# Kernel tuning notes

Measured on AMD Instinct MI355X. Metric: run time of the kernel, lower is better.

The kernel has to match this reference:

```python
import jax, jax.numpy as jnp
import numpy as np

N = 8192
E = 262144
NFEAT = 200
NHID = 128
NOUT = 16
CLUSTERS = (10, 5)


def _layernorm(x, g, b, eps=1e-5):
    mu = jnp.mean(x, axis=-1, keepdims=True)
    var = jnp.var(x, axis=-1, keepdims=True)
    return (x - mu) / jnp.sqrt(var + eps) * g + b


def _gumbel_softmax_hard(logits, g, tau=1.0):
    # straight-through gumbel softmax (hard=True), dim=1
    y = jax.nn.softmax((logits + g) / tau, axis=1)
    hard = jax.nn.one_hot(jnp.argmax(y, axis=1), y.shape[1], dtype=y.dtype)
    return hard + y - jax.lax.stop_gradient(y)


def _row_normalize(x, eps=1e-12):
    n = jnp.linalg.norm(x, axis=1, keepdims=True)
    return x / jnp.maximum(n, eps)


def setup_inputs() -> dict:
    key = jax.random.key(0)
    ks = jax.random.split(key, 20)
    u0 = jax.random.uniform(ks[3], (N, CLUSTERS[0]), minval=1e-6, maxval=1.0 - 1e-6)
    u1 = jax.random.uniform(ks[4], (CLUSTERS[0], CLUSTERS[1]), minval=1e-6, maxval=1.0 - 1e-6)
    s = 0.05
    return {
        'x': jax.random.normal(ks[0], (N, NFEAT), dtype=jnp.float32),
        'edge_index': jax.random.randint(ks[1], (2, E), 0, N, dtype=jnp.int32),
        'edge_weight': jax.random.uniform(ks[2], (E,), dtype=jnp.float32),
        'gumbel0': -jnp.log(-jnp.log(u0)),
        'gumbel1': -jnp.log(-jnp.log(u1)),
        # GCN params (2 layers, layernorm)
        'Wg1': jax.random.normal(ks[5], (NHID, NFEAT)) * s,
        'bg1': jnp.zeros((NHID,)),
        'ln1_g': jnp.ones((NHID,)), 'ln1_b': jnp.zeros((NHID,)),
        'Wg2': jax.random.normal(ks[6], (NHID, NHID)) * s,
        'bg2': jnp.zeros((NHID,)),
        'ln2_g': jnp.ones((NHID,)), 'ln2_b': jnp.zeros((NHID,)),
        # per-level pool + encoder linears
        'pool0_W': jax.random.normal(ks[7], (CLUSTERS[0], NHID)) * s,
        'pool0_b': jnp.zeros((CLUSTERS[0],)),
        'pool1_W': jax.random.normal(ks[8], (CLUSTERS[1], NHID)) * s,
        'pool1_b': jnp.zeros((CLUSTERS[1],)),
        'enc0_W': jax.random.normal(ks[9], (NHID, NHID)) * s,
        'enc0_b': jnp.zeros((NHID,)),
        'enc1_W': jax.random.normal(ks[10], (NHID, NHID)) * s,
        'enc1_b': jnp.zeros((NHID,)),
        'fc_W': jax.random.normal(ks[11], (NOUT, 3 * NHID)) * s,
        'fc_b': jnp.zeros((NOUT,)),
    }


def reference(x, edge_index, edge_weight, gumbel0, gumbel1,
              Wg1, bg1, ln1_g, ln1_b, Wg2, bg2, ln2_g, ln2_b,
              pool0_W, pool0_b, pool1_W, pool1_b,
              enc0_W, enc0_b, enc1_W, enc1_b, fc_W, fc_b):
    src, dst = edge_index[0], edge_index[1]

    def agg(h):  # weighted neighbor sum: out[i] = sum_{e: dst_e=i} w_e * h[src_e]
        return jax.ops.segment_sum(h[src] * edge_weight[:, None], dst, num_segments=N)

    # bottom GCN encoder (2 layers, layernorm)
    h = agg(x) @ Wg1.T + bg1
    h = jax.nn.relu(_layernorm(h, ln1_g, ln1_b))
    h = agg(h) @ Wg2.T + bg2
    h = _layernorm(h, ln2_g, ln2_b)
    latent = jax.nn.relu(h)  # [N, nhid]
    all_latents = [latent]

    # dense adjacency (to_dense_adj)
    adj = jnp.zeros((N, N), dtype=x.dtype).at[src, dst].add(edge_weight)

    pools = [(pool0_W, pool0_b), (pool1_W, pool1_b)]
    encs = [(enc0_W, enc0_b), (enc1_W, enc1_b)]
    gumbels = [gumbel0, gumbel1]
    product = None
    for level in range(len(CLUSTERS)):
        pW, pb = pools[level]
        eW, eb = encs[level]
        assign = _gumbel_softmax_hard(latent @ pW.T + pb, gumbels[level])  # [n_l, K]
        product = assign if level == 0 else product @ assign  # [N, K]
        xc = _row_normalize(assign.T @ latent)  # [K, nhid]
        adj = assign.T @ adj @ assign  # [K, K]
        adj = adj / jnp.sum(adj + 1e-8)
        latent = jax.nn.relu((adj @ xc) @ eW.T + eb)  # [K, nhid]
        all_latents.append(product @ latent)  # [N, nhid]

    rep = jnp.concatenate(all_latents, axis=1)  # [N, 3*nhid]
    return rep @ fc_W.T + fc_b
```

## Files before the change

### kernel.cpp

```cpp
#include <hip/hip_runtime.h>

#define N_NODES 8192
#define N_EDGES 262144
#define NFEAT 200
#define NHID 128

template<int K>
__device__ __forceinline__ void gemm_body(const float* __restrict__ A,
                                          const float* __restrict__ W,
                                          float* __restrict__ C, int bid) {
    __shared__ float a_s[8 * K];
    int row0 = bid * 8;
    const float* Ab = A + (size_t)row0 * K;
    for (int idx = threadIdx.x; idx < 8 * K; idx += 128) a_s[idx] = Ab[idx];
    __syncthreads();
    int j = threadIdx.x;
    float acc[8] = {0.f, 0.f, 0.f, 0.f, 0.f, 0.f, 0.f, 0.f};
    const float4* W4 = (const float4*)(W + (size_t)j * K);
    for (int k4 = 0; k4 < K / 4; ++k4) {
        float4 w = W4[k4];
        int k = k4 * 4;
        #pragma unroll
        for (int r = 0; r < 8; ++r) {
            const float* ar = a_s + r * K + k;
            acc[r] += ar[0] * w.x + ar[1] * w.y + ar[2] * w.z + ar[3] * w.w;
        }
    }
    #pragma unroll
    for (int r = 0; r < 8; ++r) C[(size_t)(row0 + r) * 128 + j] = acc[r];
}

template<int K>
__global__ __launch_bounds__(128) void gemm_rows(const float* __restrict__ A,
                                                 const float* __restrict__ W,
                                                 float* __restrict__ C) {
    gemm_body<K>(A, W, C, blockIdx.x);
}

__global__ __launch_bounds__(128) void gemm1_hist(const float* __restrict__ A,
                                                  const float* __restrict__ W,
                                                  float* __restrict__ C,
                                                  const int* __restrict__ ei,
                                                  int* __restrict__ deg) {
    if (blockIdx.x < N_NODES / 8) {
        gemm_body<NFEAT>(A, W, C, blockIdx.x);
    } else {
        const int* dst = ei + N_EDGES;
        for (int e = (blockIdx.x - N_NODES / 8) * 128 + threadIdx.x; e < N_EDGES; e += 64 * 128)
            atomicAdd(&deg[dst[e]], 1);
    }
}

__global__ __launch_bounds__(256) void scan_kernel(const int* __restrict__ deg,
                                                   int* __restrict__ row_start,
                                                   int* __restrict__ cursor) {
    __shared__ int part[256];
    __shared__ int partx[257];
    int tid = threadIdx.x;
    int base = tid * 32;
    int s = 0;
    for (int i = 0; i < 32; ++i) s += deg[base + i];
    part[tid] = s;
    __syncthreads();
    if (tid == 0) {
        int run = 0;
        for (int i = 0; i < 256; ++i) { partx[i] = run; run += part[i]; }
        partx[256] = run;
    }
    __syncthreads();
    int run = partx[tid];
    for (int i = 0; i < 32; ++i) {
        row_start[base + i] = run;
        cursor[base + i] = run;
        run += deg[base + i];
    }
    if (tid == 255) row_start[N_NODES] = run;
}

__global__ __launch_bounds__(256) void scatter_kernel(const int* __restrict__ ei,
                                                      const float* __restrict__ ew,
                                                      int* __restrict__ cursor,
                                                      int2* __restrict__ esort, int E) {
    int e = blockIdx.x * blockDim.x + threadIdx.x;
    if (e < E) {
        int d = ei[E + e];
        int pos = atomicAdd(&cursor[d], 1);
        esort[pos] = make_int2(ei[e], __float_as_int(ew[e]));
    }
}

__device__ __forceinline__ float2 csr_gather(const int* __restrict__ row_start,
                                             const int2* __restrict__ esort,
                                             const float* __restrict__ H,
                                             int row, int lane) {
    int s0 = row_start[row], s1 = row_start[row + 1];
    float ax0 = 0.f, ay0 = 0.f, ax1 = 0.f, ay1 = 0.f;
    float ax2 = 0.f, ay2 = 0.f, ax3 = 0.f, ay3 = 0.f;
    for (int base = s0; base < s1; base += 64) {
        int n = s1 - base;
        if (n > 64) n = 64;
        int2 meta = make_int2(0, 0);
        if (lane < n) meta = esort[base + lane];
        int k = 0;
        for (; k + 3 < n; k += 4) {
            int sA = __shfl(meta.x, k, 64);
            int sB = __shfl(meta.x, k + 1, 64);
            int sC = __shfl(meta.x, k + 2, 64);
            int sD = __shfl(meta.x, k + 3, 64);
            float wA = __int_as_float(__shfl(meta.y, k, 64));
            float wB = __int_as_float(__shfl(meta.y, k + 1, 64));
            float wC = __int_as_float(__shfl(meta.y, k + 2, 64));
            float wD = __int_as_float(__shfl(meta.y, k + 3, 64));
            float2 vA = *(const float2*)(H + (size_t)sA * 128 + lane * 2);
            float2 vB = *(const float2*)(H + (size_t)sB * 128 + lane * 2);
            float2 vC = *(const float2*)(H + (size_t)sC * 128 + lane * 2);
            float2 vD = *(const float2*)(H + (size_t)sD * 128 + lane * 2);
            ax0 += wA * vA.x; ay0 += wA * vA.y;
            ax1 += wB * vB.x; ay1 += wB * vB.y;
            ax2 += wC * vC.x; ay2 += wC * vC.y;
            ax3 += wD * vD.x; ay3 += wD * vD.y;
        }
        for (; k < n; ++k) {
            int sA = __shfl(meta.x, k, 64);
            float wA = __int_as_float(__shfl(meta.y, k, 64));
            float2 vA = *(const float2*)(H + (size_t)sA * 128 + lane * 2);
            ax0 += wA * vA.x; ay0 += wA * vA.y;
        }
    }
    return make_float2((ax0 + ax1) + (ax2 + ax3), (ay0 + ay1) + (ay2 + ay3));
}

__device__ __forceinline__ float2 ln_relu(float vx, float vy, int lane,
                                          const float* __restrict__ bias,
                                          const float* __restrict__ g,
                                          const float* __restrict__ b) {
    float2 bs = *(const float2*)(bias + lane * 2);
    vx += bs.x; vy += bs.y;
    float s = vx + vy, ss = vx * vx + vy * vy;
    for (int off = 32; off; off >>= 1) {
        s += __shfl_xor(s, off, 64);
        ss += __shfl_xor(ss, off, 64);
    }
    float mu = s * (1.f / 128.f);
    float var = ss * (1.f / 128.f) - mu * mu;
    float rs = rsqrtf(var + 1e-5f);
    float2 gg = *(const float2*)(g + lane * 2);
    float2 bb = *(const float2*)(b + lane * 2);
    return make_float2(fmaxf((vx - mu) * rs * gg.x + bb.x, 0.f),
                       fmaxf((vy - mu) * rs * gg.y + bb.y, 0.f));
}

__global__ __launch_bounds__(256) void agg_ln_csr(const int* __restrict__ row_start,
                                                  const int2* __restrict__ esort,
                                                  const float* __restrict__ H,
                                                  float* __restrict__ out,
                                                  const float* __restrict__ bias,
                                                  const float* __restrict__ g,
                                                  const float* __restrict__ b) {
    int wave = (blockIdx.x * blockDim.x + threadIdx.x) >> 6;
    int lane = threadIdx.x & 63;
    float2 a = csr_gather(row_start, esort, H, wave, lane);
    float2 y = ln_relu(a.x, a.y, lane, bias, g, b);
    *(float2*)(out + (size_t)wave * 128 + lane * 2) = y;
}

__global__ __launch_bounds__(256) void agg2_pool0(const int* __restrict__ row_start,
                                                  const int2* __restrict__ esort,
                                                  const float* __restrict__ bufC,
                                                  float* __restrict__ latent,
                                                  const float* __restrict__ bias,
                                                  const float* __restrict__ g,
                                                  const float* __restrict__ b,
                                                  const float* __restrict__ p0W,
                                                  const float* __restrict__ p0b,
                                                  const float* __restrict__ gum,
                                                  int* __restrict__ c0,
                                                  float* __restrict__ partials) {
    __shared__ float Ws[1280];
    __shared__ float accs[1280];
    __shared__ float bsh[10];
    for (int i = threadIdx.x; i < 1280; i += 256) { Ws[i] = p0W[i]; accs[i] = 0.f; }
    if (threadIdx.x < 10) bsh[threadIdx.x] = p0b[threadIdx.x];
    __syncthreads();
    int lane = threadIdx.x & 63, wid = threadIdx.x >> 6;
    int base = blockIdx.x * 16;
    for (int rr = 0; rr < 4; ++rr) {
        int row = base + rr * 4 + wid;
        float2 a = csr_gather(row_start, esort, bufC, row, lane);
        float2 y = ln_relu(a.x, a.y, lane, bias, g, b);
        *(float2*)(latent + (size_t)row * 128 + lane * 2) = y;
        float pk[10];
        #pragma unroll
        for (int k = 0; k < 10; ++k)
            pk[k] = y.x * Ws[k * 128 + lane * 2] + y.y * Ws[k * 128 + lane * 2 + 1];
        for (int off = 32; off; off >>= 1) {
            #pragma unroll
            for (int k = 0; k < 10; ++k) pk[k] += __shfl_xor(pk[k], off, 64);
        }
        const float* gr = gum + (size_t)row * 10;
        int best = 0;
        float bv = pk[0] + bsh[0] + gr[0];
        #pragma unroll
        for (int k = 1; k < 10; ++k) {
            float z = pk[k] + bsh[k] + gr[k];
            if (z > bv) { bv = z; best = k; }
        }
        if (lane == 0) c0[row] = best;
        atomicAdd(&accs[best * 128 + lane * 2], y.x);
        atomicAdd(&accs[best * 128 + lane * 2 + 1], y.y);
    }
    __syncthreads();
    for (int i = threadIdx.x; i < 1280; i += 256)
        partials[(size_t)blockIdx.x * 1280 + i] = accs[i];
}

__global__ __launch_bounds__(256) void adj_xc0(const int* __restrict__ ei,
                                               const float* __restrict__ ew,
                                               const int* __restrict__ c0,
                                               float* __restrict__ A0,
                                               const float* __restrict__ partials,
                                               float* __restrict__ xc0, int E) {
    if (blockIdx.x < 256) {
        __shared__ float As[100];
        for (int i = threadIdx.x; i < 100; i += 256) As[i] = 0.f;
        __syncthreads();
        for (int e = blockIdx.x * 256 + threadIdx.x; e < E; e += 256 * 256) {
            int a = c0[ei[e]], b = c0[ei[E + e]];
            atomicAdd(&As[a * 10 + b], ew[e]);
        }
        __syncthreads();
        for (int i = threadIdx.x; i < 100; i += 256) atomicAdd(&A0[i], As[i]);
    } else {
        int k = blockIdx.x - 256;
        int d = threadIdx.x & 127, half = threadIdx.x >> 7;
        float s0 = 0.f, s1 = 0.f, s2 = 0.f, s3 = 0.f;
        for (int b = half * 256; b < half * 256 + 256; b += 4) {
            s0 += partials[(size_t)(b    ) * 1280 + k * 128 + d];
            s1 += partials[(size_t)(b + 1) * 1280 + k * 128 + d];
            s2 += partials[(size_t)(b + 2) * 1280 + k * 128 + d];
            s3 += partials[(size_t)(b + 3) * 1280 + k * 128 + d];
        }
        __shared__ float sm[256];
        sm[threadIdx.x] = (s0 + s1) + (s2 + s3);
        __syncthreads();
        if (threadIdx.x < 128) xc0[k * 128 + d] = sm[threadIdx.x] + sm[threadIdx.x + 128];
    }
}

__global__ __launch_bounds__(256) void small_kernel(const float* __restrict__ xc0,
                                                    const float* __restrict__ A0,
                                                    const float* __restrict__ gum1,
                                                    const float* __restrict__ p1W,
                                                    const float* __restrict__ p1b,
                                                    const float* __restrict__ e0W,
                                                    const float* __restrict__ e0b,
                                                    const float* __restrict__ e1W,
                                                    const float* __restrict__ e1b,
                                                    const float* __restrict__ fcW,
                                                    const float* __restrict__ fcb,
                                                    float* __restrict__ tbl) {
    __shared__ float xc0n[10 * 128];
    __shared__ float adj0[100];
    __shared__ float m0[10 * 128];
    __shared__ float l1[10 * 128];
    __shared__ float xc1n[5 * 128];
    __shared__ float l2[5 * 128];
    __shared__ float A1[25];
    __shared__ int c1[10];
    __shared__ float red[4];

    int tid = threadIdx.x;
    int wid = tid >> 6, lane = tid & 63;

    for (int r = wid; r < 10; r += 4) {
        float2 v = *(const float2*)(xc0 + r * 128 + lane * 2);
        float ss = v.x * v.x + v.y * v.y;
        for (int off = 32; off; off >>= 1) ss += __shfl_xor(ss, off, 64);
        float sc = 1.f / fmaxf(sqrtf(ss), 1e-12f);
        xc0n[r * 128 + lane * 2] = v.x * sc;
        xc0n[r * 128 + lane * 2 + 1] = v.y * sc;
    }
    __syncthreads();
    if (tid == 0) {
        float s = 0.f;
        for (int i = 0; i < 100; ++i) s += A0[i];
        red[0] = s + 1e-6f;
    }
    __syncthreads();
    if (tid < 100) adj0[tid] = A0[tid] / red[0];
    __syncthreads();
    for (int idx = tid; idx < 1280; idx += 256) {
        int r = idx >> 7, d = idx & 127;
        float acc = 0.f;
        #pragma unroll
        for (int a = 0; a < 10; ++a) acc += adj0[r * 10 + a] * xc0n[a * 128 + d];
        m0[idx] = acc;
    }
    __syncthreads();
    for (int idx = tid; idx < 1280; idx += 256) {
        int r = idx >> 7, d = idx & 127;
        float acc = e0b[d];
        const float* wrow = e0W + d * 128;
        for (int k = 0; k < 128; ++k) acc += m0[r * 128 + k] * wrow[k];
        l1[idx] = fmaxf(acc, 0.f);
    }
    __syncthreads();
    if (tid < 10) {
        int best = 0;
        float bv = -1e30f;
        for (int j = 0; j < 5; ++j) {
            float acc = p1b[j] + gum1[tid * 5 + j];
            const float* wrow = p1W + j * 128;
            for (int k = 0; k < 128; ++k) acc += l1[tid * 128 + k] * wrow[k];
            if (acc > bv) { bv = acc; best = j; }
        }
        c1[tid] = best;
    }
    __syncthreads();
    for (int idx = tid; idx < 640; idx += 256) {
        int m = idx >> 7, d = idx & 127;
        float acc = 0.f;
        #pragma unroll
        for (int k = 0; k < 10; ++k)
            if (c1[k] == m) acc += l1[k * 128 + d];
        xc1n[idx] = acc;
    }
    __syncthreads();
    for (int r = wid; r < 5; r += 4) {
        float2 v = *(const float2*)(xc1n + r * 128 + lane * 2);
        float ss = v.x * v.x + v.y * v.y;
        for (int off = 32; off; off >>= 1) ss += __shfl_xor(ss, off, 64);
        float sc = 1.f / fmaxf(sqrtf(ss), 1e-12f);
        xc1n[r * 128 + lane * 2] = v.x * sc;
        xc1n[r * 128 + lane * 2 + 1] = v.y * sc;
    }
    __syncthreads();
    if (tid < 25) {
        int m = tid / 5, n = tid % 5;
        float acc = 0.f;
        for (int a = 0; a < 10; ++a)
            for (int b = 0; b < 10; ++b)
                if (c1[a] == m && c1[b] == n) acc += adj0[a * 10 + b];
        A1[tid] = acc;
    }
    __syncthreads();
    if (tid == 0) {
        float s = 0.f;
        for (int i = 0; i < 25; ++i) s += A1[i];
        red[1] = s + 25e-8f;
    }
    __syncthreads();
    float den1 = red[1];
    for (int idx = tid; idx < 640; idx += 256) {
        int r = idx >> 7, d = idx & 127;
        float acc = 0.f;
        #pragma unroll
        for (int a = 0; a < 5; ++a) acc += A1[r * 5 + a] * xc1n[a * 128 + d];
        m0[idx] = acc / den1;
    }
    __syncthreads();
    for (int idx = tid; idx < 640; idx += 256) {
        int r = idx >> 7, d = idx & 127;
        float acc = e1b[d];
        const float* wrow = e1W + d * 128;
        for (int k = 0; k < 128; ++k) acc += m0[r * 128 + k] * wrow[k];
        l2[idx] = fmaxf(acc, 0.f);
    }
    __syncthreads();
    for (int idx = tid; idx < 160; idx += 256) {
        int k = idx >> 4, o = idx & 15;
        float acc = fcb[o];
        const float* fB = fcW + o * 384 + 128;
        const float* fC = fcW + o * 384 + 256;
        const float* a1 = l1 + k * 128;
        const float* a2 = l2 + c1[k] * 128;
        for (int d = 0; d < 128; ++d) acc += a1[d] * fB[d] + a2[d] * fC[d];
        tbl[idx] = acc;
    }
}

__global__ __launch_bounds__(256) void out_kernel(const float* __restrict__ latent,
                                                  const int* __restrict__ c0,
                                                  const float* __restrict__ tbl,
                                                  const float* __restrict__ fcW,
                                                  float* __restrict__ out) {
    __shared__ float fA[16 * 128];
    __shared__ float ts[160];
    for (int i = threadIdx.x; i < 2048; i += 256) {
        int o = i >> 7, d = i & 127;
        fA[i] = fcW[o * 384 + d];
    }
    for (int i = threadIdx.x; i < 160; i += 256) ts[i] = tbl[i];
    __syncthreads();
    int lane = threadIdx.x & 63;
    int sub = lane & 7;
    int row = blockIdx.x * 32 + (threadIdx.x >> 6) * 8 + (lane >> 3);
    const float4* lp = (const float4*)(latent + (size_t)row * 128 + sub * 16);
    float4 x0 = lp[0], x1 = lp[1], x2 = lp[2], x3 = lp[3];
    float p[16];
    #pragma unroll
    for (int o = 0; o < 16; ++o) {
        const float4* fo = (const float4*)(fA + o * 128 + sub * 16);
        float4 w0 = fo[0], w1 = fo[1], w2 = fo[2], w3 = fo[3];
        float a = x0.x * w0.x + x0.y * w0.y + x0.z * w0.z + x0.w * w0.w;
        a += x1.x * w1.x + x1.y * w1.y + x1.z * w1.z + x1.w * w1.w;
        a += x2.x * w2.x + x2.y * w2.y + x2.z * w2.z + x2.w * w2.w;
        a += x3.x * w3.x + x3.y * w3.y + x3.z * w3.z + x3.w * w3.w;
        p[o] = a;
    }
    #pragma unroll
    for (int off = 1; off < 8; off <<= 1) {
        #pragma unroll
        for (int o = 0; o < 16; ++o) p[o] += __shfl_xor(p[o], off, 64);
    }
    int c = c0[row];
    float2 r = make_float2(p[2 * sub] + ts[c * 16 + 2 * sub],
                           p[2 * sub + 1] + ts[c * 16 + 2 * sub + 1]);
    *(float2*)(out + (size_t)row * 16 + 2 * sub) = r;
}

extern "C" void kernel_launch(void* const* d_in, const int* in_sizes, int n_in,
                              void* d_out, int out_size, void* d_ws, size_t ws_size,
                              hipStream_t stream) {
    const float* x    = (const float*)d_in[0];
    const int*   ei   = (const int*)d_in[1];
    const float* ew   = (const float*)d_in[2];
    const float* g0   = (const float*)d_in[3];
    const float* g1   = (const float*)d_in[4];
    const float* Wg1  = (const float*)d_in[5];
    const float* bg1  = (const float*)d_in[6];
    const float* ln1g = (const float*)d_in[7];
    const float* ln1b = (const float*)d_in[8];
    const float* Wg2  = (const float*)d_in[9];
    const float* bg2  = (const float*)d_in[10];
    const float* ln2g = (const float*)d_in[11];
    const float* ln2b = (const float*)d_in[12];
    const float* p0W  = (const float*)d_in[13];
    const float* p0b  = (const float*)d_in[14];
    const float* p1W  = (const float*)d_in[15];
    const float* p1b  = (const float*)d_in[16];
    const float* e0W  = (const float*)d_in[17];
    const float* e0b  = (const float*)d_in[18];
    const float* e1W  = (const float*)d_in[19];
    const float* e1b  = (const float*)d_in[20];
    const float* fcW  = (const float*)d_in[21];
    const float* fcb  = (const float*)d_in[22];
    float* out = (float*)d_out;

    float* ws   = (float*)d_ws;
    float* bufA = ws;
    float* bufB = bufA + (size_t)N_NODES * 128;
    float* bufC = bufB + (size_t)N_NODES * 128;
    int*   c0   = (int*)(bufC + (size_t)N_NODES * 128);
    float* xc0  = (float*)(c0 + N_NODES);
    float* tbl  = xc0 + 1280;
    int*   deg  = (int*)(tbl + 160);
    float* A0   = (float*)(deg + N_NODES);
    int*   row_start = (int*)(A0 + 100);
    int*   cursor    = row_start + N_NODES + 2;
    int2*  esort     = (int2*)(cursor + N_NODES);
    float* partials  = bufA;

    hipMemsetAsync(deg, 0, (N_NODES + 100) * sizeof(int), stream);

    gemm1_hist<<<N_NODES / 8 + 64, 128, 0, stream>>>(x, Wg1, bufA, ei, deg);
    scan_kernel<<<1, 256, 0, stream>>>(deg, row_start, cursor);
    scatter_kernel<<<N_EDGES / 256, 256, 0, stream>>>(ei, ew, cursor, esort, N_EDGES);

    agg_ln_csr<<<N_NODES / 4, 256, 0, stream>>>(row_start, esort, bufA, bufB,
                                                bg1, ln1g, ln1b);
    gemm_rows<NHID><<<N_NODES / 8, 128, 0, stream>>>(bufB, Wg2, bufC);

    agg2_pool0<<<512, 256, 0, stream>>>(row_start, esort, bufC, bufB,
                                        bg2, ln2g, ln2b, p0W, p0b, g0, c0, partials);

    adj_xc0<<<266, 256, 0, stream>>>(ei, ew, c0, A0, partials, xc0, N_EDGES);

    small_kernel<<<1, 256, 0, stream>>>(xc0, A0, g1, p1W, p1b, e0W, e0b, e1W, e1b,
                                        fcW, fcb, tbl);

    out_kernel<<<256, 256, 0, stream>>>(bufB, c0, tbl, fcW, out);
}
```

Measured before the change: 186.1 us.

## Stage encoder and fc weights in padded shared memory; widen pool0 blocks

The single-block small_kernel now copies the enc0, enc1, pool1 and fc weight matrices into a padded shared-memory tile before its matrix-vector products. This replaces strided global reads from one workgroup, and the pool1 logits are spread across 50 threads instead of 10. agg2_pool0 runs 1024 threads per block with one row per wave instead of a four-iteration loop over 256 threads. That exposes more concurrent gathers, but more threads now contend on the same shared atomics and the block is larger.

Measured after the change: 174.2 us. 6.4% less time.

```diff
diff --git a/kernel.cpp b/kernel.cpp
--- a/kernel.cpp
+++ b/kernel.cpp
@@ -164,53 +164,51 @@
     *(float2*)(out + (size_t)wave * 128 + lane * 2) = y;
 }
 
-__global__ __launch_bounds__(256) void agg2_pool0(const int* __restrict__ row_start,
-                                                  const int2* __restrict__ esort,
-                                                  const float* __restrict__ bufC,
-                                                  float* __restrict__ latent,
-                                                  const float* __restrict__ bias,
-                                                  const float* __restrict__ g,
-                                                  const float* __restrict__ b,
-                                                  const float* __restrict__ p0W,
-                                                  const float* __restrict__ p0b,
-                                                  const float* __restrict__ gum,
-                                                  int* __restrict__ c0,
-                                                  float* __restrict__ partials) {
+__global__ __launch_bounds__(1024) void agg2_pool0(const int* __restrict__ row_start,
+                                                   const int2* __restrict__ esort,
+                                                   const float* __restrict__ bufC,
+                                                   float* __restrict__ latent,
+                                                   const float* __restrict__ bias,
+                                                   const float* __restrict__ g,
+                                                   const float* __restrict__ b,
+                                                   const float* __restrict__ p0W,
+                                                   const float* __restrict__ p0b,
+                                                   const float* __restrict__ gum,
+                                                   int* __restrict__ c0,
+                                                   float* __restrict__ partials) {
     __shared__ float Ws[1280];
     __shared__ float accs[1280];
     __shared__ float bsh[10];
-    for (int i = threadIdx.x; i < 1280; i += 256) { Ws[i] = p0W[i]; accs[i] = 0.f; }
-    if (threadIdx.x < 10) bsh[threadIdx.x] = p0b[threadIdx.x];
-    __syncthreads();
-    int lane = threadIdx.x & 63, wid = threadIdx.x >> 6;
-    int base = blockIdx.x * 16;
-    for (int rr = 0; rr < 4; ++rr) {
-        int row = base + rr * 4 + wid;
-        float2 a = csr_gather(row_start, esort, bufC, row, lane);
-        float2 y = ln_relu(a.x, a.y, lane, bias, g, b);
-        *(float2*)(latent + (size_t)row * 128 + lane * 2) = y;
-        float pk[10];
+    int tid = threadIdx.x;
+    for (int i = tid; i < 1280; i += 1024) { Ws[i] = p0W[i]; accs[i] = 0.f; }
+    if (tid < 10) bsh[tid] = p0b[tid];
+    __syncthreads();
+    int lane = tid & 63, wid = tid >> 6;
+    int row = blockIdx.x * 16 + wid;
+    float2 a = csr_gather(row_start, esort, bufC, row, lane);
+    float2 y = ln_relu(a.x, a.y, lane, bias, g, b);
+    *(float2*)(latent + (size_t)row * 128 + lane * 2) = y;
+    float pk[10];
+    #pragma unroll
+    for (int k = 0; k < 10; ++k)
+        pk[k] = y.x * Ws[k * 128 + lane * 2] + y.y * Ws[k * 128 + lane * 2 + 1];
+    for (int off = 32; off; off >>= 1) {
         #pragma unroll
-        for (int k = 0; k < 10; ++k)
-            pk[k] = y.x * Ws[k * 128 + lane * 2] + y.y * Ws[k * 128 + lane * 2 + 1];
-        for (int off = 32; off; off >>= 1) {
-            #pragma unroll
-            for (int k = 0; k < 10; ++k) pk[k] += __shfl_xor(pk[k], off, 64);
-        }
-        const float* gr = gum + (size_t)row * 10;
-        int best = 0;
-        float bv = pk[0] + bsh[0] + gr[0];
-        #pragma unroll
-        for (int k = 1; k < 10; ++k) {
-            float z = pk[k] + bsh[k] + gr[k];
-            if (z > bv) { bv = z; best = k; }
-        }
-        if (lane == 0) c0[row] = best;
-        atomicAdd(&accs[best * 128 + lane * 2], y.x);
-        atomicAdd(&accs[best * 128 + lane * 2 + 1], y.y);
-    }
-    __syncthreads();
-    for (int i = threadIdx.x; i < 1280; i += 256)
+        for (int k = 0; k < 10; ++k) pk[k] += __shfl_xor(pk[k], off, 64);
+    }
+    const float* gr = gum + (size_t)row * 10;
+    int best = 0;
+    float bv = pk[0] + bsh[0] + gr[0];
+    #pragma unroll
+    for (int k = 1; k < 10; ++k) {
+        float z = pk[k] + bsh[k] + gr[k];
+        if (z > bv) { bv = z; best = k; }
+    }
+    if (lane == 0) c0[row] = best;
+    atomicAdd(&accs[best * 128 + lane * 2], y.x);
+    atomicAdd(&accs[best * 128 + lane * 2 + 1], y.y);
+    __syncthreads();
+    for (int i = tid; i < 1280; i += 1024)
         partials[(size_t)blockIdx.x * 1280 + i] = accs[i];
 }
 
@@ -259,6 +257,7 @@
                                                     const float* __restrict__ fcW,
                                                     const float* __restrict__ fcb,
                                                     float* __restrict__ tbl) {
+    __shared__ float Wst[64 * 129];
     __shared__ float xc0n[10 * 128];
     __shared__ float adj0[100];
     __shared__ float m0[10 * 128];
@@ -266,6 +265,7 @@
     __shared__ float xc1n[5 * 128];
     __shared__ float l2[5 * 128];
     __shared__ float A1[25];
+    __shared__ float lg[50];
     __shared__ int c1[10];
     __shared__ float red[4];
 
@@ -297,22 +297,38 @@
         m0[idx] = acc;
     }
     __syncthreads();
-    for (int idx = tid; idx < 1280; idx += 256) {
-        int r = idx >> 7, d = idx & 127;
-        float acc = e0b[d];
-        const float* wrow = e0W + d * 128;
-        for (int k = 0; k < 128; ++k) acc += m0[r * 128 + k] * wrow[k];
-        l1[idx] = fmaxf(acc, 0.f);
+    for (int h = 0; h < 2; ++h) {
+        for (int i = tid; i < 64 * 128; i += 256)
+            Wst[(i >> 7) * 129 + (i & 127)] = e0W[(size_t)(h * 64) * 128 + i];
+        __syncthreads();
+        for (int idx = tid; idx < 640; idx += 256) {
+            int r = idx >> 6, dd = idx & 63;
+            int d = h * 64 + dd;
+            float acc = e0b[d];
+            const float* wrow = Wst + dd * 129;
+            const float* mr = m0 + r * 128;
+            for (int k = 0; k < 128; ++k) acc += mr[k] * wrow[k];
+            l1[r * 128 + d] = fmaxf(acc, 0.f);
+        }
+        __syncthreads();
+    }
+    for (int i = tid; i < 640; i += 256) Wst[i] = p1W[i];
+    __syncthreads();
+    if (tid < 50) {
+        int k = tid / 5, j = tid % 5;
+        float acc = p1b[j] + gum1[k * 5 + j];
+        const float* wrow = Wst + j * 128;
+        const float* lr = l1 + k * 128;
+        for (int kk = 0; kk < 128; ++kk) acc += lr[kk] * wrow[kk];
+        lg[tid] = acc;
     }
     __syncthreads();
     if (tid < 10) {
         int best = 0;
-        float bv = -1e30f;
-        for (int j = 0; j < 5; ++j) {
-            float acc = p1b[j] + gum1[tid * 5 + j];
-            const float* wrow = p1W + j * 128;
-            for (int k = 0; k < 128; ++k) acc += l1[tid * 128 + k] * wrow[k];
-            if (acc > bv) { bv = acc; best = j; }
+        float bv = lg[tid * 5];
+        for (int j = 1; j < 5; ++j) {
+            float z = lg[tid * 5 + j];
+            if (z > bv) { bv = z; best = j; }
         }
         c1[tid] = best;
     }
@@ -359,19 +375,31 @@
         m0[idx] = acc / den1;
     }
     __syncthreads();
-    for (int idx = tid; idx < 640; idx += 256) {
-        int r = idx >> 7, d = idx & 127;
-        float acc = e1b[d];
-        const float* wrow = e1W + d * 128;
-        for (int k = 0; k < 128; ++k) acc += m0[r * 128 + k] * wrow[k];
-        l2[idx] = fmaxf(acc, 0.f);
+    for (int h = 0; h < 2; ++h) {
+        for (int i = tid; i < 64 * 128; i += 256)
+            Wst[(i >> 7) * 129 + (i & 127)] = e1W[(size_t)(h * 64) * 128 + i];
+        __syncthreads();
+        for (int idx = tid; idx < 320; idx += 256) {
+            int r = idx >> 6, dd = idx & 63;
+            int d = h * 64 + dd;
+            float acc = e1b[d];
+            const float* wrow = Wst + dd * 129;
+            const float* mr = m0 + r * 128;
+            for (int k = 0; k < 128; ++k) acc += mr[k] * wrow[k];
+            l2[r * 128 + d] = fmaxf(acc, 0.f);
+        }
+        __syncthreads();
+    }
+    for (int i = tid; i < 16 * 256; i += 256) {
+        int o = i >> 8, k2 = i & 255;
+        Wst[o * 257 + k2] = fcW[o * 384 + 128 + k2];
     }
     __syncthreads();
     for (int idx = tid; idx < 160; idx += 256) {
         int k = idx >> 4, o = idx & 15;
         float acc = fcb[o];
-        const float* fB = fcW + o * 384 + 128;
-        const float* fC = fcW + o * 384 + 256;
+        const float* fB = Wst + o * 257;
+        const float* fC = Wst + o * 257 + 128;
         const float* a1 = l1 + k * 128;
         const float* a2 = l2 + c1[k] * 128;
         for (int d = 0; d < 128; ++d) acc += a1[d] * fB[d] + a2[d] * fC[d];
@@ -471,8 +499,8 @@
                                                 bg1, ln1g, ln1b);
     gemm_rows<NHID><<<N_NODES / 8, 128, 0, stream>>>(bufB, Wg2, bufC);
 
-    agg2_pool0<<<512, 256, 0, stream>>>(row_start, esort, bufC, bufB,
-                                        bg2, ln2g, ln2b, p0W, p0b, g0, c0, partials);
+    agg2_pool0<<<512, 1024, 0, stream>>>(row_start, esort, bufC, bufB,
+                                         bg2, ln2g, ln2b, p0W, p0b, g0, c0, partials);
 
     adj_xc0<<<266, 256, 0, stream>>>(ei, ew, c0, A0, partials, xc0, N_EDGES);
 
```
